# Kernel tuning notes

Measured on AMD Instinct MI355X. Metric: run time of the kernel, lower is better.

## Reference

```python
import jax, jax.numpy as jnp
import numpy as np

INF = jnp.float32(1e12)  # stand-in for +inf in min-plus transform
ALPHA = 2.0


def _edt_sq_last(zero_mask):
    """Squared 1D euclidean distance along the last axis to the nearest True in zero_mask.

    zero_mask: bool (..., L). Returns float32 (..., L).
    """
    L = zero_mask.shape[-1]
    pos = jnp.arange(L)
    base = jnp.where(zero_mask, jnp.float32(0.0), INF)  # (..., L)

    def at(y):
        # min over y' of base[..., y'] + (y' - y)^2
        return jnp.min(base + (pos - y).astype(jnp.float32) ** 2, axis=-1)

    d = jax.lax.map(at, pos)  # (L, ...)
    return jnp.moveaxis(d, 0, -1)


def _edt_to(zero_mask):
    """Exact 2D euclidean distance to the nearest True pixel of zero_mask (..., H, W).

    Equivalent to scipy distance_transform_edt(~zero_mask): separable min-plus
    (parabola envelope) transform, pass over W then over H.
    """
    H = zero_mask.shape[-2]
    d1 = _edt_sq_last(zero_mask)  # squared dist along W: (..., H, W)
    rows = jnp.arange(H)

    def at(x):
        off = ((rows - x).astype(jnp.float32) ** 2)[:, None]  # (H, 1)
        return jnp.min(d1 + off, axis=-2)  # (..., W)

    D = jax.lax.map(at, rows)  # (H, ..., W)
    return jnp.sqrt(jnp.moveaxis(D, 0, -2))


def _distance_field(img):
    """Replicates HausdorffDTLoss.distance_field per (batch, channel) image.

    img: (B, C, H, W) float. fg = (img == 1). field = edt(fg) + edt(~fg),
    zero where the image has no foreground at all.
    """
    fg = img == jnp.float32(1.0)  # (B, C, H, W) bool
    has_fg = jnp.any(fg, axis=(-2, -1), keepdims=True)
    # scipy edt(mask) = distance to nearest zero of mask:
    fg_dist = _edt_to(~fg)  # edt(fg_mask)
    bg_dist = _edt_to(fg)   # edt(bg_mask)
    return jnp.where(has_fg, fg_dist + bg_dist, jnp.float32(0.0))


def setup_inputs() -> dict:
    key = jax.random.key(0)
    k1, k2 = jax.random.split(key)
    B, C, H, W = 4, 2, 384, 384
    pred = jax.random.uniform(k1, (B, C, H, W), dtype=jnp.float32)
    target = jax.random.randint(k2, (B, C, H, W), 0, 2).astype(jnp.float32)
    return {"pred": pred, "target": target}


def reference(pred, target):
    # distance fields are computed under no_grad in the original -> stop_gradient
    pred_dt = jax.lax.stop_gradient(_distance_field(pred))
    target_dt = jax.lax.stop_gradient(_distance_field(target))
    pred_error = (pred - target) ** 2
    distance = pred_dt ** ALPHA + target_dt ** ALPHA
    # per-channel means averaged over channels == global mean (equal counts)
    return jnp.mean(pred_error * distance)
```

## Files before the change

### kernel.cpp

```cpp
#include <hip/hip_runtime.h>
#include <stdint.h>

#define IMG_W 384
#define IMG_H 384
#define IMG_PIX (IMG_W * IMG_H)
#define N_IMG 16
#define SENT 0x7fff
#define BIGI (1 << 28)
#define GRID 1024
#define TPB 256
#define ROWS_PER_BLK 6
#define HALO 2
#define LROWS (ROWS_PER_BLK + 2 * HALO)
#define PXB (ROWS_PER_BLK * IMG_W)
#define RD_MAGIC 0x5A5AC3D0u
#define PD_MAGIC 0x3C3C96E1u

static __device__ __forceinline__ uint32_t ld_a(const uint32_t* p) {
    return __hip_atomic_load(p, __ATOMIC_RELAXED, __HIP_MEMORY_SCOPE_AGENT);
}
static __device__ __forceinline__ void st_a(uint32_t* p, uint32_t v) {
    __hip_atomic_store(p, v, __ATOMIC_RELAXED, __HIP_MEMORY_SCOPE_AGENT);
}

__device__ __forceinline__ int nearest_bit_dist(const unsigned long long m[6],
                                                int wp, int b) {
    const int BIG = 1 << 20;
    int best = BIG;
    unsigned long long t = m[wp] >> b;
    if (t) best = __builtin_ctzll(t);
#pragma unroll
    for (int w = 0; w < 6; ++w) {
        if (w > wp && m[w]) {
            int cand = ((w - wp) << 6) - b + __builtin_ctzll(m[w]);
            best = min(best, cand);
        }
    }
    unsigned long long u = m[wp] << (63 - b);
    if (u) best = min(best, (int)__builtin_clzll(u));
#pragma unroll
    for (int w = 0; w < 6; ++w) {
        if (w < wp && m[w]) {
            int cand = ((wp - w - 1) << 6) + b + 1 + __builtin_clzll(m[w]);
            best = min(best, cand);
        }
    }
    return best;
}

__global__ __launch_bounds__(TPB, 4) void k_fused(const float* __restrict__ pred,
                                                  const float* __restrict__ target,
                                                  uint32_t* __restrict__ d1,
                                                  uint32_t* __restrict__ rowdone,
                                                  uint32_t* __restrict__ partials,
                                                  uint32_t* __restrict__ pdone,
                                                  float* __restrict__ out) {
    __shared__ uint32_t lds[LROWS][IMG_W];
    __shared__ int s_ownfg;
    __shared__ int s_flag;
    __shared__ float s_part[4];

    int wave = threadIdx.x >> 6;
    int lane = threadIdx.x & 63;
    int img  = blockIdx.x >> 6;
    int chunk = blockIdx.x & 63;
    int x0 = chunk * ROWS_PER_BLK;

    if (threadIdx.x == 0) s_ownfg = 0;
    __syncthreads();

    const float* src = (img < 8) ? (pred + img * IMG_PIX)
                                 : (target + (img - 8) * IMG_PIX);

    int own_gx[2], own_fg[2], n_own = 0;
    int wave_fg = 0;
    for (int rl = wave; rl < LROWS; rl += 4) {
        int gx = x0 - HALO + rl;
        if (gx < 0 || gx >= IMG_H) {
#pragma unroll
            for (int j = 0; j < 6; ++j)
                lds[rl][lane + 64 * j] = (uint32_t)SENT | ((uint32_t)SENT << 16);
            continue;
        }
        const float* rp = src + gx * IMG_W;
        unsigned long long mf[6];
        bool any = false;
#pragma unroll
        for (int j = 0; j < 6; ++j) {
            float v = rp[lane + 64 * j];
            mf[j] = __ballot(v == 1.0f);
            any = any || (mf[j] != 0ull);
        }
        bool own = (rl >= HALO) && (rl < HALO + ROWS_PER_BLK);
        uint32_t* gdst = d1 + (size_t)(img * IMG_H + gx) * IMG_W;
        if (!any) {
#pragma unroll
            for (int j = 0; j < 6; ++j) {
                lds[rl][lane + 64 * j] = (uint32_t)SENT;
                if (own) st_a(&gdst[lane + 64 * j], (uint32_t)SENT);
            }
        } else {
            wave_fg = 1;
#pragma unroll
            for (int j = 0; j < 6; ++j) {
                bool me_fg = (mf[j] >> lane) & 1ull;
                unsigned long long sm[6];
#pragma unroll
                for (int w = 0; w < 6; ++w) sm[w] = me_fg ? ~mf[w] : mf[w];
                int dv = nearest_bit_dist(sm, j, lane);
                if (dv > SENT) dv = SENT;
                uint32_t val = me_fg ? ((uint32_t)dv << 16) : (uint32_t)dv;
                lds[rl][lane + 64 * j] = val;
                if (own) st_a(&gdst[lane + 64 * j], val);
            }
        }
        if (own) { own_gx[n_own] = gx; own_fg[n_own] = any ? 1 : 0; ++n_own; }
    }
    asm volatile("s_waitcnt vmcnt(0)" ::: "memory");
    if (lane == 0) {
        for (int i = 0; i < n_own; ++i)
            st_a(&rowdone[img * IMG_H + own_gx[i]], RD_MAGIC | (uint32_t)own_fg[i]);
        if (wave_fg) atomicOr(&s_ownfg, 1);
    }
    __syncthreads();

    bool flag;
    if (s_ownfg) {
        flag = true;
    } else {
        if (wave == 0) {
            const uint32_t* rd = rowdone + img * IMG_H;
            uint32_t fgacc = 0;
            for (;;) {
                uint32_t ok = 1; fgacc = 0;
#pragma unroll
                for (int j = 0; j < 6; ++j) {
                    uint32_t v = ld_a(&rd[lane + 64 * j]);
                    ok &= ((v & ~1u) == RD_MAGIC) ? 1u : 0u;
                    fgacc |= (v & 1u);
                }
                if (__all(ok != 0)) break;
                __builtin_amdgcn_s_sleep(2);
            }
            if (lane == 0) s_flag = __any(fgacc != 0) ? 1 : 0;
        }
        __syncthreads();
        flag = (s_flag != 0);
    }

    float contrib = 0.0f;
    if (flag) {
        const float* pp = pred   + (img & 7) * IMG_PIX;
        const float* tp = target + (img & 7) * IMG_PIX;
        float pv[9], tv[9];
#pragma unroll
        for (int t = 0; t < 9; ++t) {
            int pid = chunk * PXB + t * TPB + threadIdx.x;
            pv[t] = pp[pid];
            tv[t] = tp[pid];
        }
#pragma unroll
        for (int t = 0; t < 9; ++t) {
            int pid = chunk * PXB + t * TPB + threadIdx.x;
            int x = pid / IMG_W;
            int y = pid - x * IMG_W;
            int rl = x - x0 + HALO;
            uint32_t c0 = lds[rl][y];
            int f0 = (int)(c0 & 0xffffu), b0 = (int)(c0 >> 16);
            int bf = (f0 >= SENT) ? BIGI : f0 * f0;
            int bb = (b0 >= SENT) ? BIGI : b0 * b0;
            auto acc = [&](uint32_t cc, int kk) {
                int f = (int)(cc & 0xffffu), b2 = (int)(cc >> 16);
                if (f  < SENT) bf = min(bf, f * f + kk);
                if (b2 < SENT) bb = min(bb, b2 * b2 + kk);
            };
            acc(lds[rl - 1][y], 1); acc(lds[rl + 1][y], 1);
            acc(lds[rl - 2][y], 4); acc(lds[rl + 2][y], 4);

            int k = 3, kk = 9;
            while ((kk < bf || kk < bb) && k < IMG_H) {
                int xm = x - k, xp = x + k;
                if (xm >= 0) {
                    int xr = xm - (x0 - HALO);
                    uint32_t cc;
                    if (xr >= 0 && xr < LROWS) cc = lds[xr][y];
                    else {
                        const uint32_t* rd = &rowdone[img * IMG_H + xm];
                        while ((ld_a(rd) & ~1u) != RD_MAGIC)
                            __builtin_amdgcn_s_sleep(1);
                        cc = ld_a(&d1[(size_t)(img * IMG_H + xm) * IMG_W + y]);
                    }
                    acc(cc, kk);
                }
                if (xp < IMG_H) {
                    int xr = xp - (x0 - HALO);
                    uint32_t cc;
                    if (xr >= 0 && xr < LROWS) cc = lds[xr][y];
                    else {
                        const uint32_t* rd = &rowdone[img * IMG_H + xp];
                        while ((ld_a(rd) & ~1u) != RD_MAGIC)
                            __builtin_amdgcn_s_sleep(1);
                        cc = ld_a(&d1[(size_t)(img * IMG_H + xp) * IMG_W + y]);
                    }
                    acc(cc, kk);
                }
                ++k;
                kk = k * k;
            }
            float dbf = (bf >= BIGI) ? 1e12f : (float)bf;
            float dbb = (bb >= BIGI) ? 1e12f : (float)bb;
            float e = pv[t] - tv[t];
            contrib += e * e * (dbf + dbb);
        }
    }

    for (int o = 32; o > 0; o >>= 1) contrib += __shfl_down(contrib, o);
    if (lane == 0) s_part[wave] = contrib;
    __syncthreads();
    if (threadIdx.x == 0) {
        float s = s_part[0] + s_part[1] + s_part[2] + s_part[3];
        st_a(&partials[blockIdx.x], __float_as_uint(s));
        asm volatile("s_waitcnt vmcnt(0)" ::: "memory");
        st_a(&pdone[blockIdx.x], PD_MAGIC);
    }

    if (blockIdx.x == GRID - 1) {
        for (;;) {
            uint32_t ok = 1;
#pragma unroll
            for (int t = 0; t < 4; ++t)
                ok &= (ld_a(&pdone[threadIdx.x + 256 * t]) == PD_MAGIC) ? 1u : 0u;
            if (__syncthreads_and((int)ok)) break;
            __builtin_amdgcn_s_sleep(2);
        }
        double s = 0.0;
#pragma unroll
        for (int t = 0; t < 4; ++t)
            s += (double)__uint_as_float(ld_a(&partials[threadIdx.x + 256 * t]));
        for (int o = 32; o > 0; o >>= 1) s += __shfl_down(s, o);
        __shared__ double dpart[4];
        if (lane == 0) dpart[wave] = s;
        __syncthreads();
        if (threadIdx.x == 0)
            out[0] = (float)((dpart[0] + dpart[1] + dpart[2] + dpart[3]) *
                             (1.0 / (double)(8 * IMG_PIX)));
    }
}

extern "C" void kernel_launch(void* const* d_in, const int* in_sizes, int n_in,
                              void* d_out, int out_size, void* d_ws, size_t ws_size,
                              hipStream_t stream) {
    const float* pred   = (const float*)d_in[0];
    const float* target = (const float*)d_in[1];
    char* ws = (char*)d_ws;
    uint32_t* rowdone  = (uint32_t*)ws;
    uint32_t* pdone    = (uint32_t*)(ws + 32768);
    uint32_t* partials = (uint32_t*)(ws + 40960);
    uint32_t* d1       = (uint32_t*)(ws + 65536);

    k_fused<<<GRID, TPB, 0, stream>>>(pred, target, d1, rowdone, partials,
                                      pdone, (float*)d_out);
}
```

Before: 18.30 us.

## Drop global d1 row buffer; recompute far rows from input by direct scan

Removes the global row-distance buffer and its per-element atomic stores. Rows outside the block's halo are no longer read from other blocks' results after spinning on rowdone. Instead the needed row is scanned directly from the input, computing the nearest foreground and background distance per pixel. The row-done flag is now written per row without the store wait, and the final reduction moves to block 0. This removes global writes and inter-block dependency waits, but a far-row lookup now costs a full 384-element scan instead of one load. Those lookups are rare for random binary inputs.

```diff
diff --git a/kernel.cpp b/kernel.cpp
--- a/kernel.cpp
+++ b/kernel.cpp
@@ -50,7 +50,6 @@
 
 __global__ __launch_bounds__(TPB, 4) void k_fused(const float* __restrict__ pred,
                                                   const float* __restrict__ target,
-                                                  uint32_t* __restrict__ d1,
                                                   uint32_t* __restrict__ rowdone,
                                                   uint32_t* __restrict__ partials,
                                                   uint32_t* __restrict__ pdone,
@@ -60,9 +59,9 @@
     __shared__ int s_flag;
     __shared__ float s_part[4];
 
-    int wave = threadIdx.x >> 6;
-    int lane = threadIdx.x & 63;
-    int img  = blockIdx.x >> 6;
+    int wave  = threadIdx.x >> 6;
+    int lane  = threadIdx.x & 63;
+    int img   = blockIdx.x >> 6;
     int chunk = blockIdx.x & 63;
     int x0 = chunk * ROWS_PER_BLK;
 
@@ -72,7 +71,6 @@
     const float* src = (img < 8) ? (pred + img * IMG_PIX)
                                  : (target + (img - 8) * IMG_PIX);
 
-    int own_gx[2], own_fg[2], n_own = 0;
     int wave_fg = 0;
     for (int rl = wave; rl < LROWS; rl += 4) {
         int gx = x0 - HALO + rl;
@@ -92,13 +90,9 @@
             any = any || (mf[j] != 0ull);
         }
         bool own = (rl >= HALO) && (rl < HALO + ROWS_PER_BLK);
-        uint32_t* gdst = d1 + (size_t)(img * IMG_H + gx) * IMG_W;
         if (!any) {
 #pragma unroll
-            for (int j = 0; j < 6; ++j) {
-                lds[rl][lane + 64 * j] = (uint32_t)SENT;
-                if (own) st_a(&gdst[lane + 64 * j], (uint32_t)SENT);
-            }
+            for (int j = 0; j < 6; ++j) lds[rl][lane + 64 * j] = (uint32_t)SENT;
         } else {
             wave_fg = 1;
 #pragma unroll
@@ -109,19 +103,13 @@
                 for (int w = 0; w < 6; ++w) sm[w] = me_fg ? ~mf[w] : mf[w];
                 int dv = nearest_bit_dist(sm, j, lane);
                 if (dv > SENT) dv = SENT;
-                uint32_t val = me_fg ? ((uint32_t)dv << 16) : (uint32_t)dv;
-                lds[rl][lane + 64 * j] = val;
-                if (own) st_a(&gdst[lane + 64 * j], val);
+                lds[rl][lane + 64 * j] = me_fg ? ((uint32_t)dv << 16) : (uint32_t)dv;
             }
         }
-        if (own) { own_gx[n_own] = gx; own_fg[n_own] = any ? 1 : 0; ++n_own; }
-    }
-    asm volatile("s_waitcnt vmcnt(0)" ::: "memory");
-    if (lane == 0) {
-        for (int i = 0; i < n_own; ++i)
-            st_a(&rowdone[img * IMG_H + own_gx[i]], RD_MAGIC | (uint32_t)own_fg[i]);
-        if (wave_fg) atomicOr(&s_ownfg, 1);
-    }
+        if (own && lane == 0)
+            st_a(&rowdone[img * IMG_H + gx], RD_MAGIC | (any ? 1u : 0u));
+    }
+    if (lane == 0 && wave_fg) atomicOr(&s_ownfg, 1);
     __syncthreads();
 
     bool flag;
@@ -174,6 +162,17 @@
                 if (f  < SENT) bf = min(bf, f * f + kk);
                 if (b2 < SENT) bb = min(bb, b2 * b2 + kk);
             };
+            auto far_acc = [&](int gx, int kk) {
+                const float* frow = src + gx * IMG_W;
+                int df = BIGI, db = BIGI;
+                for (int yp = 0; yp < IMG_W; ++yp) {
+                    int dd = (yp > y) ? (yp - y) : (y - yp);
+                    if (frow[yp] == 1.0f) df = min(df, dd);
+                    else                  db = min(db, dd);
+                }
+                if (df < BIGI) bf = min(bf, df * df + kk);
+                if (db < BIGI) bb = min(bb, db * db + kk);
+            };
             acc(lds[rl - 1][y], 1); acc(lds[rl + 1][y], 1);
             acc(lds[rl - 2][y], 4); acc(lds[rl + 2][y], 4);
 
@@ -182,27 +181,13 @@
                 int xm = x - k, xp = x + k;
                 if (xm >= 0) {
                     int xr = xm - (x0 - HALO);
-                    uint32_t cc;
-                    if (xr >= 0 && xr < LROWS) cc = lds[xr][y];
-                    else {
-                        const uint32_t* rd = &rowdone[img * IMG_H + xm];
-                        while ((ld_a(rd) & ~1u) != RD_MAGIC)
-                            __builtin_amdgcn_s_sleep(1);
-                        cc = ld_a(&d1[(size_t)(img * IMG_H + xm) * IMG_W + y]);
-                    }
-                    acc(cc, kk);
+                    if (xr >= 0 && xr < LROWS) acc(lds[xr][y], kk);
+                    else                       far_acc(xm, kk);
                 }
                 if (xp < IMG_H) {
                     int xr = xp - (x0 - HALO);
-                    uint32_t cc;
-                    if (xr >= 0 && xr < LROWS) cc = lds[xr][y];
-                    else {
-                        const uint32_t* rd = &rowdone[img * IMG_H + xp];
-                        while ((ld_a(rd) & ~1u) != RD_MAGIC)
-                            __builtin_amdgcn_s_sleep(1);
-                        cc = ld_a(&d1[(size_t)(img * IMG_H + xp) * IMG_W + y]);
-                    }
-                    acc(cc, kk);
+                    if (xr >= 0 && xr < LROWS) acc(lds[xr][y], kk);
+                    else                       far_acc(xp, kk);
                 }
                 ++k;
                 kk = k * k;
@@ -224,7 +209,7 @@
         st_a(&pdone[blockIdx.x], PD_MAGIC);
     }
 
-    if (blockIdx.x == GRID - 1) {
+    if (blockIdx.x == 0) {
         for (;;) {
             uint32_t ok = 1;
 #pragma unroll
@@ -256,8 +241,7 @@
     uint32_t* rowdone  = (uint32_t*)ws;
     uint32_t* pdone    = (uint32_t*)(ws + 32768);
     uint32_t* partials = (uint32_t*)(ws + 40960);
-    uint32_t* d1       = (uint32_t*)(ws + 65536);
-
-    k_fused<<<GRID, TPB, 0, stream>>>(pred, target, d1, rowdone, partials,
+
+    k_fused<<<GRID, TPB, 0, stream>>>(pred, target, rowdone, partials,
                                       pdone, (float*)d_out);
 }
```

Result: faster. 17.24 us (-5.8%).
